# Kernel tuning notes

Hardware: AMD Instinct MI355X
Metric: run time of the kernel (lower is better)

Reference implementation:

```python
import jax, jax.numpy as jnp
import numpy as np

IN_DIM = 784
HIDDEN = 512
STYLE = 128
BATCH = 2048
NUM_LABELS = 10


def setup_inputs() -> dict:
    key = jax.random.key(0)
    k1, k2, k3, k4 = jax.random.split(key, 4)
    x = jax.random.uniform(k1, (BATCH, IN_DIM), dtype=jnp.float32)
    m = jax.random.randint(k2, (BATCH,), 0, NUM_LABELS)
    # Embedding tables, scaled as in the torch __init__ (N(0,1)/fan)
    fc1_table = jax.random.normal(k3, (NUM_LABELS, (IN_DIM + 1) * HIDDEN), dtype=jnp.float32) / ((IN_DIM + 1) * HIDDEN)
    fc2_table = jax.random.normal(k4, (NUM_LABELS, (HIDDEN + 1) * STYLE), dtype=jnp.float32) / ((HIDDEN + 1) * STYLE)
    return {"x": x, "m": m, "fc1_table": fc1_table, "fc2_table": fc2_table}


def reference(x, m, fc1_table, fc2_table):
    B = x.shape[0]
    x = x.reshape(B, -1)  # [B, 784]
    # Per-sample weight matrices gathered by label
    fc1 = fc1_table[m].reshape(B, IN_DIM + 1, HIDDEN)   # [B, 785, H]
    fc1_w, fc1_b = fc1[:, :IN_DIM, :], fc1[:, -1, :]
    h1 = jax.nn.relu(jnp.einsum('bkj,bk->bj', fc1_w, x) + fc1_b)  # [B, H]
    fc2 = fc2_table[m].reshape(B, HIDDEN + 1, STYLE)    # [B, H+1, S]
    fc2_w, fc2_b = fc2[:, :HIDDEN, :], fc2[:, -1, :]
    h2 = jnp.einsum('bkj,bk->bj', fc2_w, h1) + fc2_b    # [B, S]
    return jax.nn.sigmoid(h2)
```

## Files before the change

kernel.cpp:

```cpp
#include <hip/hip_runtime.h>
#include <hip/hip_bf16.h>
#include <math.h>

#define BATCH      2048
#define IN_DIM     784
#define HIDDEN     512
#define STYLE      128
#define NUM_LABELS 10
#define FC1_STRIDE ((IN_DIM + 1) * HIDDEN)
#define FC2_STRIDE ((HIDDEN + 1) * STYLE)
#define KP1        832
#define TB         64
#define BK         64
#define MAX_TILES  48

#define META_NTILES 31
#define META_TILES  32
#define META_PERM   176

#define W1B_OFF  16384ULL
#define W2B_OFF  (W1B_OFF + 10ULL*HIDDEN*KP1*2)
#define H1B_OFF  (W2B_OFF + 10ULL*STYLE*HIDDEN*2)
#define BF16_NEED (H1B_OFF + (size_t)BATCH*HIDDEN*2)

#define W1T_K  (KP1/64)
#define W1T_N  (HIDDEN/64)
#define W2T_K  (HIDDEN/64)
#define W2T_N  (STYLE/64)
#define W1_TBLK (W1T_K*W1T_N*NUM_LABELS)
#define W2_TBLK (W2T_K*W2T_N*NUM_LABELS)

typedef short short8  __attribute__((ext_vector_type(8)));
typedef float float4e __attribute__((ext_vector_type(4)));

__device__ __forceinline__ ushort f2b(float v) {
    __hip_bfloat16 h = __float2bfloat16(v);
    return *reinterpret_cast<ushort*>(&h);
}

__global__ void k_prep(const int* __restrict__ m, const float* __restrict__ fc1t,
                       const float* __restrict__ fc2t, int* __restrict__ meta,
                       ushort* __restrict__ w1b, ushort* __restrict__ w2b) {
    const int tid = threadIdx.x;
    int bid = blockIdx.x;

    __shared__ int cnt[NUM_LABELS], curs[NUM_LABELS], offs[NUM_LABELS + 1];
    __shared__ int permS[BATCH];
    __shared__ float tile[64][68];

    if (bid == 0) {
        if (tid < NUM_LABELS) { cnt[tid] = 0; curs[tid] = 0; }
        __syncthreads();
        for (int b = tid; b < BATCH; b += 256) atomicAdd(&cnt[m[b]], 1);
        __syncthreads();
        if (tid == 0) {
            int off = 0;
            for (int L = 0; L < NUM_LABELS; ++L) { offs[L] = off; off += cnt[L]; }
            offs[NUM_LABELS] = off;
        }
        __syncthreads();
        for (int b = tid; b < BATCH; b += 256) {
            int L = m[b];
            int r = atomicAdd(&curs[L], 1);
            permS[offs[L] + r] = b;
        }
        __syncthreads();
        for (int i = tid; i < BATCH; i += 256) meta[META_PERM + i] = permS[i];
        if (tid == 0) {
            int idx = 0;
            for (int L = 0; L < NUM_LABELS; ++L) {
                int c = cnt[L], off = offs[L];
                for (int t = 0; t < c; t += TB) {
                    meta[META_TILES + idx * 3 + 0] = L;
                    meta[META_TILES + idx * 3 + 1] = off + t;
                    meta[META_TILES + idx * 3 + 2] = min(TB, c - t);
                    ++idx;
                }
            }
            meta[META_NTILES] = idx;
        }
        return;
    }

    bid -= 1;
    const float* src; ushort* dst; int Kv, Kp, N, kb, nb, L; size_t sL, dL;
    if (bid < W1_TBLK) {
        kb = bid % W1T_K; nb = (bid / W1T_K) % W1T_N; L = bid / (W1T_K * W1T_N);
        src = fc1t; dst = w1b; Kv = IN_DIM; Kp = KP1; N = HIDDEN;
        sL = FC1_STRIDE; dL = (size_t)HIDDEN * KP1;
    } else {
        int q2 = bid - W1_TBLK;
        kb = q2 % W2T_K; nb = (q2 / W2T_K) % W2T_N; L = q2 / (W2T_K * W2T_N);
        src = fc2t; dst = w2b; Kv = HIDDEN; Kp = HIDDEN; N = STYLE;
        sL = FC2_STRIDE; dL = (size_t)STYLE * HIDDEN;
    }
    const int k0 = kb * 64, n0 = nb * 64;
    const int r = tid >> 2, q = tid & 3;
    const int gk = k0 + r;
#pragma unroll
    for (int j = 0; j < 4; ++j) {
        float4 v = make_float4(0.f, 0.f, 0.f, 0.f);
        if (gk < Kv) v = *(const float4*)(src + (size_t)L * sL + (size_t)gk * N + n0 + q * 16 + j * 4);
        *(float4*)&tile[r][q * 16 + j * 4] = v;
    }
    __syncthreads();
    const int n = tid >> 2;
    ushort kv[16];
#pragma unroll
    for (int j = 0; j < 16; ++j) kv[j] = f2b(tile[q * 16 + j][n]);
    ushort* drow = dst + (size_t)L * dL + (size_t)(n0 + n) * Kp + k0 + q * 16;
    *(uint4*)(drow + 0) = *(const uint4*)&kv[0];
    *(uint4*)(drow + 8) = *(const uint4*)&kv[8];
}

__launch_bounds__(256)
__global__ void k_fc1m(const float* __restrict__ x, const ushort* __restrict__ w1b,
                       const float* __restrict__ fc1t, const int* __restrict__ meta,
                       ushort* __restrict__ h1b) {
    const int t = blockIdx.x;
    if (t >= meta[META_NTILES]) return;
    const int L      = meta[META_TILES + 3 * t + 0];
    const int pstart = meta[META_TILES + 3 * t + 1];
    const int nrows  = meta[META_TILES + 3 * t + 2];
    const int col0   = blockIdx.y * 64;
    const ushort* __restrict__ W = w1b + (size_t)L * HIDDEN * KP1 + (size_t)col0 * KP1;

    __shared__ int rows[TB];
    __shared__ __align__(16) ushort As[2][64][72];
    __shared__ __align__(16) ushort Bs[2][64][72];

    const int tid = threadIdx.x;
    if (tid < TB) rows[tid] = (tid < nrows) ? meta[META_PERM + pstart + tid] : -1;
    __syncthreads();

    const int sr = tid >> 2, sc = tid & 3;
    const int lane = tid & 63, wv = tid >> 6;
    const int qd = lane >> 4, ln16 = lane & 15;

    const int arow = rows[sr];
    const float* __restrict__ xr = x + (size_t)(arow < 0 ? 0 : arow) * IN_DIM;
    const uint4* __restrict__ bgp = (const uint4*)(W + (size_t)sr * KP1);

    float4e acc[4] = {};
    float4 a0, a1, a2, a3;
    uint4 b0, b1;

    {
        const int ka = sc * 16;
        a0 = make_float4(0.f,0.f,0.f,0.f); a1 = a0; a2 = a0; a3 = a0;
        if (arow >= 0) {
            if (ka      < IN_DIM) a0 = *(const float4*)(xr + ka);
            if (ka + 4  < IN_DIM) a1 = *(const float4*)(xr + ka + 4);
            if (ka + 8  < IN_DIM) a2 = *(const float4*)(xr + ka + 8);
            if (ka + 12 < IN_DIM) a3 = *(const float4*)(xr + ka + 12);
        }
        b0 = bgp[sc * 2 + 0];
        b1 = bgp[sc * 2 + 1];
        ushort av[16];
        av[0]=f2b(a0.x); av[1]=f2b(a0.y); av[2]=f2b(a0.z); av[3]=f2b(a0.w);
        av[4]=f2b(a1.x); av[5]=f2b(a1.y); av[6]=f2b(a1.z); av[7]=f2b(a1.w);
        av[8]=f2b(a2.x); av[9]=f2b(a2.y); av[10]=f2b(a2.z); av[11]=f2b(a2.w);
        av[12]=f2b(a3.x); av[13]=f2b(a3.y); av[14]=f2b(a3.z); av[15]=f2b(a3.w);
        *(uint4*)&As[0][sr][sc * 16 + 0] = *(const uint4*)&av[0];
        *(uint4*)&As[0][sr][sc * 16 + 8] = *(const uint4*)&av[8];
        *(uint4*)&Bs[0][sr][sc * 16 + 0] = b0;
        *(uint4*)&Bs[0][sr][sc * 16 + 8] = b1;
    }
    {
        const int ka = BK + sc * 16;
        a0 = make_float4(0.f,0.f,0.f,0.f); a1 = a0; a2 = a0; a3 = a0;
        if (arow >= 0) {
            if (ka      < IN_DIM) a0 = *(const float4*)(xr + ka);
            if (ka + 4  < IN_DIM) a1 = *(const float4*)(xr + ka + 4);
            if (ka + 8  < IN_DIM) a2 = *(const float4*)(xr + ka + 8);
            if (ka + 12 < IN_DIM) a3 = *(const float4*)(xr + ka + 12);
        }
        b0 = bgp[(BK >> 3) + sc * 2 + 0];
        b1 = bgp[(BK >> 3) + sc * 2 + 1];
    }

    int p = 0;
    for (int k0 = 0; k0 < KP1; k0 += BK) {
        __syncthreads();
        if (k0 + BK < KP1) {
            ushort av[16];
            av[0]=f2b(a0.x); av[1]=f2b(a0.y); av[2]=f2b(a0.z); av[3]=f2b(a0.w);
            av[4]=f2b(a1.x); av[5]=f2b(a1.y); av[6]=f2b(a1.z); av[7]=f2b(a1.w);
            av[8]=f2b(a2.x); av[9]=f2b(a2.y); av[10]=f2b(a2.z); av[11]=f2b(a2.w);
            av[12]=f2b(a3.x); av[13]=f2b(a3.y); av[14]=f2b(a3.z); av[15]=f2b(a3.w);
            *(uint4*)&As[1-p][sr][sc * 16 + 0] = *(const uint4*)&av[0];
            *(uint4*)&As[1-p][sr][sc * 16 + 8] = *(const uint4*)&av[8];
            *(uint4*)&Bs[1-p][sr][sc * 16 + 0] = b0;
            *(uint4*)&Bs[1-p][sr][sc * 16 + 8] = b1;
        }
        if (k0 + 2*BK < KP1) {
            const int ka = k0 + 2*BK + sc * 16;
            a0 = make_float4(0.f,0.f,0.f,0.f); a1 = a0; a2 = a0; a3 = a0;
            if (arow >= 0) {
                if (ka      < IN_DIM) a0 = *(const float4*)(xr + ka);
                if (ka + 4  < IN_DIM) a1 = *(const float4*)(xr + ka + 4);
                if (ka + 8  < IN_DIM) a2 = *(const float4*)(xr + ka + 8);
                if (ka + 12 < IN_DIM) a3 = *(const float4*)(xr + ka + 12);
            }
            b0 = bgp[((k0 + 2*BK) >> 3) + sc * 2 + 0];
            b1 = bgp[((k0 + 2*BK) >> 3) + sc * 2 + 1];
        }
#pragma unroll
        for (int s = 0; s < 2; ++s) {
            short8 af = *(const short8*)&As[p][wv * 16 + ln16][s * 32 + qd * 8];
#pragma unroll
            for (int nt = 0; nt < 4; ++nt) {
                short8 bf = *(const short8*)&Bs[p][nt * 16 + ln16][s * 32 + qd * 8];
                acc[nt] = __builtin_amdgcn_mfma_f32_16x16x32_bf16(af, bf, acc[nt], 0, 0, 0);
            }
        }
        p ^= 1;
    }

    const float* __restrict__ bias = fc1t + (size_t)L * FC1_STRIDE + (size_t)IN_DIM * HIDDEN + col0;
#pragma unroll
    for (int nt = 0; nt < 4; ++nt) {
        const int c = nt * 16 + ln16;
        const float bs = bias[c];
#pragma unroll
        for (int i = 0; i < 4; ++i) {
            const int r = wv * 16 + qd * 4 + i;
            if (r < nrows)
                h1b[(size_t)(pstart + r) * HIDDEN + col0 + c] = f2b(fmaxf(acc[nt][i] + bs, 0.f));
        }
    }
}

__launch_bounds__(256)
__global__ void k_fc2m(const ushort* __restrict__ h1b, const ushort* __restrict__ w2b,
                       const float* __restrict__ fc2t, const int* __restrict__ meta,
                       float* __restrict__ out) {
    const int t = blockIdx.x;
    if (t >= meta[META_NTILES]) return;
    const int L      = meta[META_TILES + 3 * t + 0];
    const int pstart = meta[META_TILES + 3 * t + 1];
    const int nrows  = meta[META_TILES + 3 * t + 2];
    const int col0   = blockIdx.y * 64;
    const ushort* __restrict__ W = w2b + (size_t)L * STYLE * HIDDEN + (size_t)col0 * HIDDEN;

    __shared__ int rows[TB];
    __shared__ __align__(16) ushort As[2][64][72];
    __shared__ __align__(16) ushort Bs[2][64][72];

    const int tid = threadIdx.x;
    if (tid < TB) rows[tid] = (tid < nrows) ? meta[META_PERM + pstart + tid] : -1;
    __syncthreads();

    const int sr = tid >> 2, sc = tid & 3;
    const int lane = tid & 63, wv = tid >> 6;
    const int qd = lane >> 4, ln16 = lane & 15;

    const bool aval = (sr < nrows);
    const uint4* __restrict__ agp = (const uint4*)(h1b + (size_t)(pstart + (aval ? sr : 0)) * HIDDEN);
    const uint4* __restrict__ bgp = (const uint4*)(W + (size_t)sr * HIDDEN);

    float4e acc[4] = {};
    uint4 a0, a1, b0, b1;

    a0 = make_uint4(0u,0u,0u,0u); a1 = a0;
    if (aval) { a0 = agp[sc * 2 + 0]; a1 = agp[sc * 2 + 1]; }
    b0 = bgp[sc * 2 + 0];
    b1 = bgp[sc * 2 + 1];
    *(uint4*)&As[0][sr][sc * 16 + 0] = a0;
    *(uint4*)&As[0][sr][sc * 16 + 8] = a1;
    *(uint4*)&Bs[0][sr][sc * 16 + 0] = b0;
    *(uint4*)&Bs[0][sr][sc * 16 + 8] = b1;
    {
        const int base = (BK >> 3) + sc * 2;
        a0 = make_uint4(0u,0u,0u,0u); a1 = a0;
        if (aval) { a0 = agp[base]; a1 = agp[base + 1]; }
        b0 = bgp[base];
        b1 = bgp[base + 1];
    }

    int p = 0;
    for (int k0 = 0; k0 < HIDDEN; k0 += BK) {
        __syncthreads();
        if (k0 + BK < HIDDEN) {
            *(uint4*)&As[1-p][sr][sc * 16 + 0] = a0;
            *(uint4*)&As[1-p][sr][sc * 16 + 8] = a1;
            *(uint4*)&Bs[1-p][sr][sc * 16 + 0] = b0;
            *(uint4*)&Bs[1-p][sr][sc * 16 + 8] = b1;
        }
        if (k0 + 2*BK < HIDDEN) {
            const int base = ((k0 + 2*BK) >> 3) + sc * 2;
            a0 = make_uint4(0u,0u,0u,0u); a1 = a0;
            if (aval) { a0 = agp[base]; a1 = agp[base + 1]; }
            b0 = bgp[base];
            b1 = bgp[base + 1];
        }
#pragma unroll
        for (int s = 0; s < 2; ++s) {
            short8 af = *(const short8*)&As[p][wv * 16 + ln16][s * 32 + qd * 8];
#pragma unroll
            for (int nt = 0; nt < 4; ++nt) {
                short8 bf = *(const short8*)&Bs[p][nt * 16 + ln16][s * 32 + qd * 8];
                acc[nt] = __builtin_amdgcn_mfma_f32_16x16x32_bf16(af, bf, acc[nt], 0, 0, 0);
            }
        }
        p ^= 1;
    }

    const float* __restrict__ bias = fc2t + (size_t)L * FC2_STRIDE + (size_t)HIDDEN * STYLE + col0;
#pragma unroll
    for (int nt = 0; nt < 4; ++nt) {
        const int c = nt * 16 + ln16;
        const float bs = bias[c];
#pragma unroll
        for (int i = 0; i < 4; ++i) {
            const int r = wv * 16 + qd * 4 + i;
            if (r < nrows) {
                const int orow = rows[r];
                out[(size_t)orow * STYLE + col0 + c] = 1.f / (1.f + __expf(-(acc[nt][i] + bs)));
            }
        }
    }
}

__launch_bounds__(256)
__global__ void k_naive(const float* __restrict__ x, const int* __restrict__ m,
                        const float* __restrict__ fc1t, const float* __restrict__ fc2t,
                        float* __restrict__ out) {
    __shared__ float xs[IN_DIM];
    __shared__ float h1[HIDDEN];
    const int b = blockIdx.x, tid = threadIdx.x, L = m[b];
    for (int k = tid; k < IN_DIM; k += 256) xs[k] = x[(size_t)b * IN_DIM + k];
    __syncthreads();
    const float* __restrict__ W1 = fc1t + (size_t)L * FC1_STRIDE;
    for (int j = tid; j < HIDDEN; j += 256) {
        float acc = W1[(size_t)IN_DIM * HIDDEN + j];
        for (int k = 0; k < IN_DIM; ++k) acc = fmaf(xs[k], W1[(size_t)k * HIDDEN + j], acc);
        h1[j] = fmaxf(acc, 0.f);
    }
    __syncthreads();
    const float* __restrict__ W2 = fc2t + (size_t)L * FC2_STRIDE;
    for (int j = tid; j < STYLE; j += 256) {
        float acc = W2[(size_t)HIDDEN * STYLE + j];
        for (int k = 0; k < HIDDEN; ++k) acc = fmaf(h1[k], W2[(size_t)k * STYLE + j], acc);
        out[(size_t)b * STYLE + j] = 1.f / (1.f + __expf(-acc));
    }
}

extern "C" void kernel_launch(void* const* d_in, const int* in_sizes, int n_in,
                              void* d_out, int out_size, void* d_ws, size_t ws_size,
                              hipStream_t stream) {
    const float* x    = (const float*)d_in[0];
    const int*   m    = (const int*)d_in[1];
    const float* fc1t = (const float*)d_in[2];
    const float* fc2t = (const float*)d_in[3];
    float* out = (float*)d_out;

    if (ws_size >= BF16_NEED) {
        int*    meta = (int*)d_ws;
        ushort* w1b  = (ushort*)((char*)d_ws + W1B_OFF);
        ushort* w2b  = (ushort*)((char*)d_ws + W2B_OFF);
        ushort* h1b  = (ushort*)((char*)d_ws + H1B_OFF);

        k_prep<<<1 + W1_TBLK + W2_TBLK, 256, 0, stream>>>(m, fc1t, fc2t, meta, w1b, w2b);
        k_fc1m<<<dim3(MAX_TILES, HIDDEN / 64), 256, 0, stream>>>(x, w1b, fc1t, meta, h1b);
        k_fc2m<<<dim3(MAX_TILES, STYLE / 64), 256, 0, stream>>>(h1b, w2b, fc2t, meta, out);
    } else {
        k_naive<<<BATCH, 256, 0, stream>>>(x, m, fc1t, fc2t, out);
    }
}
```

Before: 102.3 us.

## Fuse fc1 and fc2 GEMM kernels with per-tile atomic flag handoff

Merges the two GEMM launches into one grid where blockIdx.y 0-7 compute fc1 column blocks and 8-9 compute fc2 for the same row tile. The fc2 blocks spin on per-tile global counters, using an epoch scheme, until all eight fc1 producers for their tile have written h1. The aim is to drop one kernel launch and let fc2 for early tiles overlap with fc1 for later tiles. It relies on every producer block eventually being scheduled while consumers spin; the grid is small enough that all blocks should be co-resident, but this is not guaranteed and could deadlock.

```diff
diff --git a/kernel.cpp b/kernel.cpp
--- a/kernel.cpp
+++ b/kernel.cpp
@@ -33,6 +33,9 @@
 typedef short short8  __attribute__((ext_vector_type(8)));
 typedef float float4e __attribute__((ext_vector_type(4)));
 
+__device__ int g_flag[MAX_TILES * 8];
+__device__ int g_cons[MAX_TILES * 2];
+
 __device__ __forceinline__ ushort f2b(float v) {
     __hip_bfloat16 h = __float2bfloat16(v);
     return *reinterpret_cast<ushort*>(&h);
@@ -114,16 +117,16 @@
 }
 
 __launch_bounds__(256)
-__global__ void k_fc1m(const float* __restrict__ x, const ushort* __restrict__ w1b,
-                       const float* __restrict__ fc1t, const int* __restrict__ meta,
-                       ushort* __restrict__ h1b) {
+__global__ void k_fused(const float* __restrict__ x, const ushort* __restrict__ w1b,
+                        const ushort* __restrict__ w2b, const float* __restrict__ fc1t,
+                        const float* __restrict__ fc2t, const int* __restrict__ meta,
+                        ushort* __restrict__ h1b, float* __restrict__ out) {
     const int t = blockIdx.x;
+    const int role = blockIdx.y;
     if (t >= meta[META_NTILES]) return;
     const int L      = meta[META_TILES + 3 * t + 0];
     const int pstart = meta[META_TILES + 3 * t + 1];
     const int nrows  = meta[META_TILES + 3 * t + 2];
-    const int col0   = blockIdx.y * 64;
-    const ushort* __restrict__ W = w1b + (size_t)L * HIDDEN * KP1 + (size_t)col0 * KP1;
 
     __shared__ int rows[TB];
     __shared__ __align__(16) ushort As[2][64][72];
@@ -137,64 +140,18 @@
     const int lane = tid & 63, wv = tid >> 6;
     const int qd = lane >> 4, ln16 = lane & 15;
 
-    const int arow = rows[sr];
-    const float* __restrict__ xr = x + (size_t)(arow < 0 ? 0 : arow) * IN_DIM;
-    const uint4* __restrict__ bgp = (const uint4*)(W + (size_t)sr * KP1);
-
-    float4e acc[4] = {};
-    float4 a0, a1, a2, a3;
-    uint4 b0, b1;
-
-    {
-        const int ka = sc * 16;
-        a0 = make_float4(0.f,0.f,0.f,0.f); a1 = a0; a2 = a0; a3 = a0;
-        if (arow >= 0) {
-            if (ka      < IN_DIM) a0 = *(const float4*)(xr + ka);
-            if (ka + 4  < IN_DIM) a1 = *(const float4*)(xr + ka + 4);
-            if (ka + 8  < IN_DIM) a2 = *(const float4*)(xr + ka + 8);
-            if (ka + 12 < IN_DIM) a3 = *(const float4*)(xr + ka + 12);
-        }
-        b0 = bgp[sc * 2 + 0];
-        b1 = bgp[sc * 2 + 1];
-        ushort av[16];
-        av[0]=f2b(a0.x); av[1]=f2b(a0.y); av[2]=f2b(a0.z); av[3]=f2b(a0.w);
-        av[4]=f2b(a1.x); av[5]=f2b(a1.y); av[6]=f2b(a1.z); av[7]=f2b(a1.w);
-        av[8]=f2b(a2.x); av[9]=f2b(a2.y); av[10]=f2b(a2.z); av[11]=f2b(a2.w);
-        av[12]=f2b(a3.x); av[13]=f2b(a3.y); av[14]=f2b(a3.z); av[15]=f2b(a3.w);
-        *(uint4*)&As[0][sr][sc * 16 + 0] = *(const uint4*)&av[0];
-        *(uint4*)&As[0][sr][sc * 16 + 8] = *(const uint4*)&av[8];
-        *(uint4*)&Bs[0][sr][sc * 16 + 0] = b0;
-        *(uint4*)&Bs[0][sr][sc * 16 + 8] = b1;
-    }
-    {
-        const int ka = BK + sc * 16;
-        a0 = make_float4(0.f,0.f,0.f,0.f); a1 = a0; a2 = a0; a3 = a0;
-        if (arow >= 0) {
-            if (ka      < IN_DIM) a0 = *(const float4*)(xr + ka);
-            if (ka + 4  < IN_DIM) a1 = *(const float4*)(xr + ka + 4);
-            if (ka + 8  < IN_DIM) a2 = *(const float4*)(xr + ka + 8);
-            if (ka + 12 < IN_DIM) a3 = *(const float4*)(xr + ka + 12);
-        }
-        b0 = bgp[(BK >> 3) + sc * 2 + 0];
-        b1 = bgp[(BK >> 3) + sc * 2 + 1];
-    }
-
-    int p = 0;
-    for (int k0 = 0; k0 < KP1; k0 += BK) {
-        __syncthreads();
-        if (k0 + BK < KP1) {
-            ushort av[16];
-            av[0]=f2b(a0.x); av[1]=f2b(a0.y); av[2]=f2b(a0.z); av[3]=f2b(a0.w);
-            av[4]=f2b(a1.x); av[5]=f2b(a1.y); av[6]=f2b(a1.z); av[7]=f2b(a1.w);
-            av[8]=f2b(a2.x); av[9]=f2b(a2.y); av[10]=f2b(a2.z); av[11]=f2b(a2.w);
-            av[12]=f2b(a3.x); av[13]=f2b(a3.y); av[14]=f2b(a3.z); av[15]=f2b(a3.w);
-            *(uint4*)&As[1-p][sr][sc * 16 + 0] = *(const uint4*)&av[0];
-            *(uint4*)&As[1-p][sr][sc * 16 + 8] = *(const uint4*)&av[8];
-            *(uint4*)&Bs[1-p][sr][sc * 16 + 0] = b0;
-            *(uint4*)&Bs[1-p][sr][sc * 16 + 8] = b1;
-        }
-        if (k0 + 2*BK < KP1) {
-            const int ka = k0 + 2*BK + sc * 16;
+    if (role < 8) {
+        const int col0 = role * 64;
+        const ushort* __restrict__ W = w1b + (size_t)L * HIDDEN * KP1 + (size_t)col0 * KP1;
+        const int arow = rows[sr];
+        const float* __restrict__ xr = x + (size_t)(arow < 0 ? 0 : arow) * IN_DIM;
+        const uint4* __restrict__ bgp = (const uint4*)(W + (size_t)sr * KP1);
+
+        float4e acc[4] = {};
+        float4 a0, a1, a2, a3;
+        uint4 b0, b1;
+        {
+            const int ka = sc * 16;
             a0 = make_float4(0.f,0.f,0.f,0.f); a1 = a0; a2 = a0; a3 = a0;
             if (arow >= 0) {
                 if (ka      < IN_DIM) a0 = *(const float4*)(xr + ka);
@@ -202,121 +159,165 @@
                 if (ka + 8  < IN_DIM) a2 = *(const float4*)(xr + ka + 8);
                 if (ka + 12 < IN_DIM) a3 = *(const float4*)(xr + ka + 12);
             }
-            b0 = bgp[((k0 + 2*BK) >> 3) + sc * 2 + 0];
-            b1 = bgp[((k0 + 2*BK) >> 3) + sc * 2 + 1];
-        }
-#pragma unroll
-        for (int s = 0; s < 2; ++s) {
-            short8 af = *(const short8*)&As[p][wv * 16 + ln16][s * 32 + qd * 8];
-#pragma unroll
-            for (int nt = 0; nt < 4; ++nt) {
-                short8 bf = *(const short8*)&Bs[p][nt * 16 + ln16][s * 32 + qd * 8];
-                acc[nt] = __builtin_amdgcn_mfma_f32_16x16x32_bf16(af, bf, acc[nt], 0, 0, 0);
-            }
-        }
-        p ^= 1;
-    }
-
-    const float* __restrict__ bias = fc1t + (size_t)L * FC1_STRIDE + (size_t)IN_DIM * HIDDEN + col0;
-#pragma unroll
-    for (int nt = 0; nt < 4; ++nt) {
-        const int c = nt * 16 + ln16;
-        const float bs = bias[c];
-#pragma unroll
-        for (int i = 0; i < 4; ++i) {
-            const int r = wv * 16 + qd * 4 + i;
-            if (r < nrows)
-                h1b[(size_t)(pstart + r) * HIDDEN + col0 + c] = f2b(fmaxf(acc[nt][i] + bs, 0.f));
-        }
-    }
-}
-
-__launch_bounds__(256)
-__global__ void k_fc2m(const ushort* __restrict__ h1b, const ushort* __restrict__ w2b,
-                       const float* __restrict__ fc2t, const int* __restrict__ meta,
-                       float* __restrict__ out) {
-    const int t = blockIdx.x;
-    if (t >= meta[META_NTILES]) return;
-    const int L      = meta[META_TILES + 3 * t + 0];
-    const int pstart = meta[META_TILES + 3 * t + 1];
-    const int nrows  = meta[META_TILES + 3 * t + 2];
-    const int col0   = blockIdx.y * 64;
-    const ushort* __restrict__ W = w2b + (size_t)L * STYLE * HIDDEN + (size_t)col0 * HIDDEN;
-
-    __shared__ int rows[TB];
-    __shared__ __align__(16) ushort As[2][64][72];
-    __shared__ __align__(16) ushort Bs[2][64][72];
-
-    const int tid = threadIdx.x;
-    if (tid < TB) rows[tid] = (tid < nrows) ? meta[META_PERM + pstart + tid] : -1;
-    __syncthreads();
-
-    const int sr = tid >> 2, sc = tid & 3;
-    const int lane = tid & 63, wv = tid >> 6;
-    const int qd = lane >> 4, ln16 = lane & 15;
-
-    const bool aval = (sr < nrows);
-    const uint4* __restrict__ agp = (const uint4*)(h1b + (size_t)(pstart + (aval ? sr : 0)) * HIDDEN);
-    const uint4* __restrict__ bgp = (const uint4*)(W + (size_t)sr * HIDDEN);
-
-    float4e acc[4] = {};
-    uint4 a0, a1, b0, b1;
-
-    a0 = make_uint4(0u,0u,0u,0u); a1 = a0;
-    if (aval) { a0 = agp[sc * 2 + 0]; a1 = agp[sc * 2 + 1]; }
-    b0 = bgp[sc * 2 + 0];
-    b1 = bgp[sc * 2 + 1];
-    *(uint4*)&As[0][sr][sc * 16 + 0] = a0;
-    *(uint4*)&As[0][sr][sc * 16 + 8] = a1;
-    *(uint4*)&Bs[0][sr][sc * 16 + 0] = b0;
-    *(uint4*)&Bs[0][sr][sc * 16 + 8] = b1;
-    {
-        const int base = (BK >> 3) + sc * 2;
+            b0 = bgp[sc * 2 + 0];
+            b1 = bgp[sc * 2 + 1];
+            ushort av[16];
+            av[0]=f2b(a0.x); av[1]=f2b(a0.y); av[2]=f2b(a0.z); av[3]=f2b(a0.w);
+            av[4]=f2b(a1.x); av[5]=f2b(a1.y); av[6]=f2b(a1.z); av[7]=f2b(a1.w);
+            av[8]=f2b(a2.x); av[9]=f2b(a2.y); av[10]=f2b(a2.z); av[11]=f2b(a2.w);
+            av[12]=f2b(a3.x); av[13]=f2b(a3.y); av[14]=f2b(a3.z); av[15]=f2b(a3.w);
+            *(uint4*)&As[0][sr][sc * 16 + 0] = *(const uint4*)&av[0];
+            *(uint4*)&As[0][sr][sc * 16 + 8] = *(const uint4*)&av[8];
+            *(uint4*)&Bs[0][sr][sc * 16 + 0] = b0;
+            *(uint4*)&Bs[0][sr][sc * 16 + 8] = b1;
+        }
+        {
+            const int ka = BK + sc * 16;
+            a0 = make_float4(0.f,0.f,0.f,0.f); a1 = a0; a2 = a0; a3 = a0;
+            if (arow >= 0) {
+                if (ka      < IN_DIM) a0 = *(const float4*)(xr + ka);
+                if (ka + 4  < IN_DIM) a1 = *(const float4*)(xr + ka + 4);
+                if (ka + 8  < IN_DIM) a2 = *(const float4*)(xr + ka + 8);
+                if (ka + 12 < IN_DIM) a3 = *(const float4*)(xr + ka + 12);
+            }
+            b0 = bgp[(BK >> 3) + sc * 2 + 0];
+            b1 = bgp[(BK >> 3) + sc * 2 + 1];
+        }
+
+        int p = 0;
+        for (int k0 = 0; k0 < KP1; k0 += BK) {
+            __syncthreads();
+            if (k0 + BK < KP1) {
+                ushort av[16];
+                av[0]=f2b(a0.x); av[1]=f2b(a0.y); av[2]=f2b(a0.z); av[3]=f2b(a0.w);
+                av[4]=f2b(a1.x); av[5]=f2b(a1.y); av[6]=f2b(a1.z); av[7]=f2b(a1.w);
+                av[8]=f2b(a2.x); av[9]=f2b(a2.y); av[10]=f2b(a2.z); av[11]=f2b(a2.w);
+                av[12]=f2b(a3.x); av[13]=f2b(a3.y); av[14]=f2b(a3.z); av[15]=f2b(a3.w);
+                *(uint4*)&As[1-p][sr][sc * 16 + 0] = *(const uint4*)&av[0];
+                *(uint4*)&As[1-p][sr][sc * 16 + 8] = *(const uint4*)&av[8];
+                *(uint4*)&Bs[1-p][sr][sc * 16 + 0] = b0;
+                *(uint4*)&Bs[1-p][sr][sc * 16 + 8] = b1;
+            }
+            if (k0 + 2*BK < KP1) {
+                const int ka = k0 + 2*BK + sc * 16;
+                a0 = make_float4(0.f,0.f,0.f,0.f); a1 = a0; a2 = a0; a3 = a0;
+                if (arow >= 0) {
+                    if (ka      < IN_DIM) a0 = *(const float4*)(xr + ka);
+                    if (ka + 4  < IN_DIM) a1 = *(const float4*)(xr + ka + 4);
+                    if (ka + 8  < IN_DIM) a2 = *(const float4*)(xr + ka + 8);
+                    if (ka + 12 < IN_DIM) a3 = *(const float4*)(xr + ka + 12);
+                }
+                b0 = bgp[((k0 + 2*BK) >> 3) + sc * 2 + 0];
+                b1 = bgp[((k0 + 2*BK) >> 3) + sc * 2 + 1];
+            }
+#pragma unroll
+            for (int s = 0; s < 2; ++s) {
+                short8 af = *(const short8*)&As[p][wv * 16 + ln16][s * 32 + qd * 8];
+#pragma unroll
+                for (int nt = 0; nt < 4; ++nt) {
+                    short8 bf = *(const short8*)&Bs[p][nt * 16 + ln16][s * 32 + qd * 8];
+                    acc[nt] = __builtin_amdgcn_mfma_f32_16x16x32_bf16(af, bf, acc[nt], 0, 0, 0);
+                }
+            }
+            p ^= 1;
+        }
+
+        const float* __restrict__ bias = fc1t + (size_t)L * FC1_STRIDE + (size_t)IN_DIM * HIDDEN + col0;
+#pragma unroll
+        for (int nt = 0; nt < 4; ++nt) {
+            const int c = nt * 16 + ln16;
+            const float bs = bias[c];
+#pragma unroll
+            for (int i = 0; i < 4; ++i) {
+                const int r = wv * 16 + qd * 4 + i;
+                if (r < nrows)
+                    h1b[(size_t)(pstart + r) * HIDDEN + col0 + c] = f2b(fmaxf(acc[nt][i] + bs, 0.f));
+            }
+        }
+        __syncthreads();
+        if (tid == 0) {
+            __threadfence();
+            __hip_atomic_fetch_add(&g_flag[t * 8 + role], 1, __ATOMIC_RELAXED,
+                                   __HIP_MEMORY_SCOPE_AGENT);
+        }
+    } else {
+        const int cb = role - 8;
+        const int col0 = cb * 64;
+        if (tid == 0) {
+            int ep = __hip_atomic_fetch_add(&g_cons[t * 2 + cb], 1, __ATOMIC_RELAXED,
+                                            __HIP_MEMORY_SCOPE_AGENT);
+            const int target = ep + 1;
+            for (int i = 0; i < 8; ++i)
+                while (__hip_atomic_load(&g_flag[t * 8 + i], __ATOMIC_RELAXED,
+                                         __HIP_MEMORY_SCOPE_AGENT) < target)
+                    __builtin_amdgcn_s_sleep(8);
+        }
+        __syncthreads();
+        __threadfence();
+
+        const ushort* __restrict__ W = w2b + (size_t)L * STYLE * HIDDEN + (size_t)col0 * HIDDEN;
+        const bool aval = (sr < nrows);
+        const uint4* __restrict__ agp = (const uint4*)(h1b + (size_t)(pstart + (aval ? sr : 0)) * HIDDEN);
+        const uint4* __restrict__ bgp = (const uint4*)(W + (size_t)sr * HIDDEN);
+
+        float4e acc[4] = {};
+        uint4 a0, a1, b0, b1;
         a0 = make_uint4(0u,0u,0u,0u); a1 = a0;
-        if (aval) { a0 = agp[base]; a1 = agp[base + 1]; }
-        b0 = bgp[base];
-        b1 = bgp[base + 1];
-    }
-
-    int p = 0;
-    for (int k0 = 0; k0 < HIDDEN; k0 += BK) {
-        __syncthreads();
-        if (k0 + BK < HIDDEN) {
-            *(uint4*)&As[1-p][sr][sc * 16 + 0] = a0;
-            *(uint4*)&As[1-p][sr][sc * 16 + 8] = a1;
-            *(uint4*)&Bs[1-p][sr][sc * 16 + 0] = b0;
-            *(uint4*)&Bs[1-p][sr][sc * 16 + 8] = b1;
-        }
-        if (k0 + 2*BK < HIDDEN) {
-            const int base = ((k0 + 2*BK) >> 3) + sc * 2;
+        if (aval) { a0 = agp[sc * 2 + 0]; a1 = agp[sc * 2 + 1]; }
+        b0 = bgp[sc * 2 + 0];
+        b1 = bgp[sc * 2 + 1];
+        *(uint4*)&As[0][sr][sc * 16 + 0] = a0;
+        *(uint4*)&As[0][sr][sc * 16 + 8] = a1;
+        *(uint4*)&Bs[0][sr][sc * 16 + 0] = b0;
+        *(uint4*)&Bs[0][sr][sc * 16 + 8] = b1;
+        {
+            const int base = (BK >> 3) + sc * 2;
             a0 = make_uint4(0u,0u,0u,0u); a1 = a0;
             if (aval) { a0 = agp[base]; a1 = agp[base + 1]; }
             b0 = bgp[base];
             b1 = bgp[base + 1];
         }
-#pragma unroll
-        for (int s = 0; s < 2; ++s) {
-            short8 af = *(const short8*)&As[p][wv * 16 + ln16][s * 32 + qd * 8];
-#pragma unroll
-            for (int nt = 0; nt < 4; ++nt) {
-                short8 bf = *(const short8*)&Bs[p][nt * 16 + ln16][s * 32 + qd * 8];
-                acc[nt] = __builtin_amdgcn_mfma_f32_16x16x32_bf16(af, bf, acc[nt], 0, 0, 0);
-            }
-        }
-        p ^= 1;
-    }
-
-    const float* __restrict__ bias = fc2t + (size_t)L * FC2_STRIDE + (size_t)HIDDEN * STYLE + col0;
-#pragma unroll
-    for (int nt = 0; nt < 4; ++nt) {
-        const int c = nt * 16 + ln16;
-        const float bs = bias[c];
-#pragma unroll
-        for (int i = 0; i < 4; ++i) {
-            const int r = wv * 16 + qd * 4 + i;
-            if (r < nrows) {
-                const int orow = rows[r];
-                out[(size_t)orow * STYLE + col0 + c] = 1.f / (1.f + __expf(-(acc[nt][i] + bs)));
+
+        int p = 0;
+        for (int k0 = 0; k0 < HIDDEN; k0 += BK) {
+            __syncthreads();
+            if (k0 + BK < HIDDEN) {
+                *(uint4*)&As[1-p][sr][sc * 16 + 0] = a0;
+                *(uint4*)&As[1-p][sr][sc * 16 + 8] = a1;
+                *(uint4*)&Bs[1-p][sr][sc * 16 + 0] = b0;
+                *(uint4*)&Bs[1-p][sr][sc * 16 + 8] = b1;
+            }
+            if (k0 + 2*BK < HIDDEN) {
+                const int base = ((k0 + 2*BK) >> 3) + sc * 2;
+                a0 = make_uint4(0u,0u,0u,0u); a1 = a0;
+                if (aval) { a0 = agp[base]; a1 = agp[base + 1]; }
+                b0 = bgp[base];
+                b1 = bgp[base + 1];
+            }
+#pragma unroll
+            for (int s = 0; s < 2; ++s) {
+                short8 af = *(const short8*)&As[p][wv * 16 + ln16][s * 32 + qd * 8];
+#pragma unroll
+                for (int nt = 0; nt < 4; ++nt) {
+                    short8 bf = *(const short8*)&Bs[p][nt * 16 + ln16][s * 32 + qd * 8];
+                    acc[nt] = __builtin_amdgcn_mfma_f32_16x16x32_bf16(af, bf, acc[nt], 0, 0, 0);
+                }
+            }
+            p ^= 1;
+        }
+
+        const float* __restrict__ bias = fc2t + (size_t)L * FC2_STRIDE + (size_t)HIDDEN * STYLE + col0;
+#pragma unroll
+        for (int nt = 0; nt < 4; ++nt) {
+            const int c = nt * 16 + ln16;
+            const float bs = bias[c];
+#pragma unroll
+            for (int i = 0; i < 4; ++i) {
+                const int r = wv * 16 + qd * 4 + i;
+                if (r < nrows) {
+                    const int orow = rows[r];
+                    out[(size_t)orow * STYLE + col0 + c] = 1.f / (1.f + __expf(-(acc[nt][i] + bs)));
+                }
             }
         }
     }
@@ -362,8 +363,7 @@
         ushort* h1b  = (ushort*)((char*)d_ws + H1B_OFF);
 
         k_prep<<<1 + W1_TBLK + W2_TBLK, 256, 0, stream>>>(m, fc1t, fc2t, meta, w1b, w2b);
-        k_fc1m<<<dim3(MAX_TILES, HIDDEN / 64), 256, 0, stream>>>(x, w1b, fc1t, meta, h1b);
-        k_fc2m<<<dim3(MAX_TILES, STYLE / 64), 256, 0, stream>>>(h1b, w2b, fc2t, meta, out);
+        k_fused<<<dim3(MAX_TILES, 10), 256, 0, stream>>>(x, w1b, w2b, fc1t, fc2t, meta, h1b, out);
     } else {
         k_naive<<<BATCH, 256, 0, stream>>>(x, m, fc1t, fc2t, out);
     }
```

After: 115.4 us. +12.8%, slower.

## Compute per-block label tiling inside GEMM kernels instead of a serial prep block

Applied to the files above, without the earlier changes.

Removes the single-block label sort from k_prep, where one thread serially built the tile list and the permutation in global meta. Each GEMM block now loads all labels itself, counts them with ballot/popcount, finds its tile and does a block-wide prefix scan to collect its row indices in shared memory. This takes the serial prep block off the critical path and drops the meta round-trip through global memory. In exchange every GEMM block, including idle ones, redoes the label counting and scan.

```diff
diff --git a/kernel.cpp b/kernel.cpp
--- a/kernel.cpp
+++ b/kernel.cpp
@@ -14,11 +14,7 @@
 #define BK         64
 #define MAX_TILES  48
 
-#define META_NTILES 31
-#define META_TILES  32
-#define META_PERM   176
-
-#define W1B_OFF  16384ULL
+#define W1B_OFF  0ULL
 #define W2B_OFF  (W1B_OFF + 10ULL*HIDDEN*KP1*2)
 #define H1B_OFF  (W2B_OFF + 10ULL*STYLE*HIDDEN*2)
 #define BF16_NEED (H1B_OFF + (size_t)BATCH*HIDDEN*2)
@@ -38,51 +34,77 @@
     return *reinterpret_cast<ushort*>(&h);
 }
 
-__global__ void k_prep(const int* __restrict__ m, const float* __restrict__ fc1t,
-                       const float* __restrict__ fc2t, int* __restrict__ meta,
+__device__ __forceinline__ bool block_meta(const int* __restrict__ m, int bt,
+                                           int* cntS, int* scanS, int* rowsS,
+                                           int& L, int& pstart, int& nrows) {
+    const int tid = threadIdx.x;
+    int mloc[8];
+#pragma unroll
+    for (int i = 0; i < 8; ++i) mloc[i] = m[tid * 8 + i];
+
+    if (tid < NUM_LABELS) cntS[tid] = 0;
+    __syncthreads();
+#pragma unroll
+    for (int i = 0; i < 8; ++i) {
+        const int v = mloc[i];
+#pragma unroll
+        for (int Li = 0; Li < NUM_LABELS; ++Li) {
+            unsigned long long bal = __ballot(v == Li);
+            if ((tid & 63) == 0) atomicAdd(&cntS[Li], (int)__popcll(bal));
+        }
+    }
+    __syncthreads();
+
+    L = -1; pstart = 0; nrows = 0; int t = 0;
+    {
+        int off = 0, idx = 0;
+        for (int Li = 0; Li < NUM_LABELS; ++Li) {
+            const int c = cntS[Li];
+            const int nt = (c + TB - 1) >> 6;
+            if (L < 0 && bt >= idx && bt < idx + nt) {
+                L = Li; t = bt - idx;
+                pstart = off + t * TB;
+                nrows = min(TB, c - t * TB);
+            }
+            idx += nt; off += c;
+        }
+    }
+    if (L < 0) return false;
+
+    int loc = 0;
+#pragma unroll
+    for (int i = 0; i < 8; ++i) loc += (mloc[i] == L);
+    scanS[tid] = loc;
+    __syncthreads();
+    for (int s = 1; s < 256; s <<= 1) {
+        int v = scanS[tid];
+        int u = (tid >= s) ? scanS[tid - s] : 0;
+        __syncthreads();
+        scanS[tid] = v + u;
+        __syncthreads();
+    }
+    const int base = (tid > 0) ? scanS[tid - 1] : 0;
+    if (tid < TB) rowsS[tid] = -1;
+    __syncthreads();
+    const int lo = t * TB, hi = lo + TB;
+    int r = base;
+#pragma unroll
+    for (int i = 0; i < 8; ++i) {
+        if (mloc[i] == L) {
+            if (r >= lo && r < hi) rowsS[r - lo] = tid * 8 + i;
+            ++r;
+        }
+    }
+    __syncthreads();
+    return true;
+}
+
+__global__ void k_prep(const float* __restrict__ fc1t, const float* __restrict__ fc2t,
                        ushort* __restrict__ w1b, ushort* __restrict__ w2b) {
     const int tid = threadIdx.x;
     int bid = blockIdx.x;
-
-    __shared__ int cnt[NUM_LABELS], curs[NUM_LABELS], offs[NUM_LABELS + 1];
-    __shared__ int permS[BATCH];
     __shared__ float tile[64][68];
 
-    if (bid == 0) {
-        if (tid < NUM_LABELS) { cnt[tid] = 0; curs[tid] = 0; }
-        __syncthreads();
-        for (int b = tid; b < BATCH; b += 256) atomicAdd(&cnt[m[b]], 1);
-        __syncthreads();
-        if (tid == 0) {
-            int off = 0;
-            for (int L = 0; L < NUM_LABELS; ++L) { offs[L] = off; off += cnt[L]; }
-            offs[NUM_LABELS] = off;
-        }
-        __syncthreads();
-        for (int b = tid; b < BATCH; b += 256) {
-            int L = m[b];
-            int r = atomicAdd(&curs[L], 1);
-            permS[offs[L] + r] = b;
-        }
-        __syncthreads();
-        for (int i = tid; i < BATCH; i += 256) meta[META_PERM + i] = permS[i];
-        if (tid == 0) {
-            int idx = 0;
-            for (int L = 0; L < NUM_LABELS; ++L) {
-                int c = cnt[L], off = offs[L];
-                for (int t = 0; t < c; t += TB) {
-                    meta[META_TILES + idx * 3 + 0] = L;
-                    meta[META_TILES + idx * 3 + 1] = off + t;
-                    meta[META_TILES + idx * 3 + 2] = min(TB, c - t);
-                    ++idx;
-                }
-            }
-            meta[META_NTILES] = idx;
-        }
-        return;
-    }
-
-    bid -= 1;
     const float* src; ushort* dst; int Kv, Kp, N, kb, nb, L; size_t sL, dL;
     if (bid < W1_TBLK) {
         kb = bid % W1T_K; nb = (bid / W1T_K) % W1T_N; L = bid / (W1T_K * W1T_N);
@@ -114,25 +136,19 @@
 }
 
 __launch_bounds__(256)
-__global__ void k_fc1m(const float* __restrict__ x, const ushort* __restrict__ w1b,
-                       const float* __restrict__ fc1t, const int* __restrict__ meta,
+__global__ void k_fc1m(const float* __restrict__ x, const int* __restrict__ m,
+                       const ushort* __restrict__ w1b, const float* __restrict__ fc1t,
                        ushort* __restrict__ h1b) {
-    const int t = blockIdx.x;
-    if (t >= meta[META_NTILES]) return;
-    const int L      = meta[META_TILES + 3 * t + 0];
-    const int pstart = meta[META_TILES + 3 * t + 1];
-    const int nrows  = meta[META_TILES + 3 * t + 2];
-    const int col0   = blockIdx.y * 64;
-    const ushort* __restrict__ W = w1b + (size_t)L * HIDDEN * KP1 + (size_t)col0 * KP1;
-
-    __shared__ int rows[TB];
+    __shared__ int cntS[NUM_LABELS], scanS[256], rows[TB];
     __shared__ __align__(16) ushort As[2][64][72];
     __shared__ __align__(16) ushort Bs[2][64][72];
 
+    int L, pstart, nrows;
+    if (!block_meta(m, blockIdx.x, cntS, scanS, rows, L, pstart, nrows)) return;
+    const int col0 = blockIdx.y * 64;
+    const ushort* __restrict__ W = w1b + (size_t)L * HIDDEN * KP1 + (size_t)col0 * KP1;
+
     const int tid = threadIdx.x;
-    if (tid < TB) rows[tid] = (tid < nrows) ? meta[META_PERM + pstart + tid] : -1;
-    __syncthreads();
-
     const int sr = tid >> 2, sc = tid & 3;
     const int lane = tid & 63, wv = tid >> 6;
     const int qd = lane >> 4, ln16 = lane & 15;
@@ -232,25 +248,19 @@
 }
 
 __launch_bounds__(256)
-__global__ void k_fc2m(const ushort* __restrict__ h1b, const ushort* __restrict__ w2b,
-                       const float* __restrict__ fc2t, const int* __restrict__ meta,
+__global__ void k_fc2m(const ushort* __restrict__ h1b, const int* __restrict__ m,
+                       const ushort* __restrict__ w2b, const float* __restrict__ fc2t,
                        float* __restrict__ out) {
-    const int t = blockIdx.x;
-    if (t >= meta[META_NTILES]) return;
-    const int L      = meta[META_TILES + 3 * t + 0];
-    const int pstart = meta[META_TILES + 3 * t + 1];
-    const int nrows  = meta[META_TILES + 3 * t + 2];
-    const int col0   = blockIdx.y * 64;
-    const ushort* __restrict__ W = w2b + (size_t)L * STYLE * HIDDEN + (size_t)col0 * HIDDEN;
-
-    __shared__ int rows[TB];
+    __shared__ int cntS[NUM_LABELS], scanS[256], rows[TB];
     __shared__ __align__(16) ushort As[2][64][72];
     __shared__ __align__(16) ushort Bs[2][64][72];
 
+    int L, pstart, nrows;
+    if (!block_meta(m, blockIdx.x, cntS, scanS, rows, L, pstart, nrows)) return;
+    const int col0 = blockIdx.y * 64;
+    const ushort* __restrict__ W = w2b + (size_t)L * STYLE * HIDDEN + (size_t)col0 * HIDDEN;
+
     const int tid = threadIdx.x;
-    if (tid < TB) rows[tid] = (tid < nrows) ? meta[META_PERM + pstart + tid] : -1;
-    __syncthreads();
-
     const int sr = tid >> 2, sc = tid & 3;
     const int lane = tid & 63, wv = tid >> 6;
     const int qd = lane >> 4, ln16 = lane & 15;
@@ -356,14 +366,13 @@
     float* out = (float*)d_out;
 
     if (ws_size >= BF16_NEED) {
-        int*    meta = (int*)d_ws;
-        ushort* w1b  = (ushort*)((char*)d_ws + W1B_OFF);
-        ushort* w2b  = (ushort*)((char*)d_ws + W2B_OFF);
-        ushort* h1b  = (ushort*)((char*)d_ws + H1B_OFF);
-
-        k_prep<<<1 + W1_TBLK + W2_TBLK, 256, 0, stream>>>(m, fc1t, fc2t, meta, w1b, w2b);
-        k_fc1m<<<dim3(MAX_TILES, HIDDEN / 64), 256, 0, stream>>>(x, w1b, fc1t, meta, h1b);
-        k_fc2m<<<dim3(MAX_TILES, STYLE / 64), 256, 0, stream>>>(h1b, w2b, fc2t, meta, out);
+        ushort* w1b = (ushort*)((char*)d_ws + W1B_OFF);
+        ushort* w2b = (ushort*)((char*)d_ws + W2B_OFF);
+        ushort* h1b = (ushort*)((char*)d_ws + H1B_OFF);
+
+        k_prep<<<W1_TBLK + W2_TBLK, 256, 0, stream>>>(fc1t, fc2t, w1b, w2b);
+        k_fc1m<<<dim3(MAX_TILES, HIDDEN / 64), 256, 0, stream>>>(x, m, w1b, fc1t, h1b);
+        k_fc2m<<<dim3(MAX_TILES, STYLE / 64), 256, 0, stream>>>(h1b, m, w2b, fc2t, out);
     } else {
         k_naive<<<BATCH, 256, 0, stream>>>(x, m, fc1t, fc2t, out);
     }
```

Result: slower. 113.7 us (+11.2%).
